# Optimization experiments

Hardware: AMD Instinct MI355X
Metric: run time of the kernel (lower is better)

Reference implementation:

```python
import jax, jax.numpy as jnp
import numpy as np

B, TQ, TKV, D, H = 2, 1024, 1024, 1024, 16
HD = D // H
BUCKETS, MAX_REL = 32, 128
SPAN = BUCKETS  # pos_ebd_size


def make_log_bucket_position(rel_pos, bucket_size, max_position):
    sign = jnp.sign(rel_pos)
    mid = bucket_size // 2
    abs_pos = jnp.where((rel_pos < mid) & (rel_pos > -mid), mid - 1, jnp.abs(rel_pos))
    log_pos = jnp.ceil(jnp.log(abs_pos.astype(jnp.float32) / mid)
                       / np.float32(np.log((max_position - 1) / mid)) * (mid - 1)) + mid
    return jnp.where(abs_pos <= mid, rel_pos, (log_pos * sign).astype(rel_pos.dtype))


def setup_inputs():
    key = jax.random.key(0)
    ks = jax.random.split(key, 12)
    s = 0.02
    f32 = jnp.float32
    return {
        "query_states": jax.random.normal(ks[0], (B, TQ, D), f32),
        "key_value_states": jax.random.normal(ks[1], (B, TKV, D), f32),
        "Wq": jax.random.normal(ks[2], (D, D), f32) * s, "bq": jnp.zeros((D,), f32),
        "Wk": jax.random.normal(ks[3], (D, D), f32) * s, "bk": jnp.zeros((D,), f32),
        "Wv": jax.random.normal(ks[4], (D, D), f32) * s, "bv": jnp.zeros((D,), f32),
        "Wo": jax.random.normal(ks[5], (D, D), f32) * s, "bo": jnp.zeros((D,), f32),
        "Wpk": jax.random.normal(ks[6], (D, D), f32) * s, "bpk": jnp.zeros((D,), f32),
        "Wpq": jax.random.normal(ks[7], (D, D), f32) * s, "bpq": jnp.zeros((D,), f32),
        "rel_emb": jax.random.normal(ks[8], (2 * SPAN, D), f32) * s,
        "ln_g": jnp.ones((D,), f32), "ln_b": jnp.zeros((D,), f32),
        "attention_mask": jnp.zeros((B, TKV), jnp.bool_),
    }


def reference(query_states, key_value_states, Wq, bq, Wk, bk, Wv, bv, Wo, bo,
              Wpk, bpk, Wpq, bpq, rel_emb, ln_g, ln_b, attention_mask):
    # projections -> [B,H,T,hd]
    q = (query_states @ Wq.T + bq).reshape(B, TQ, H, HD).transpose(0, 2, 1, 3)
    k = (key_value_states @ Wk.T + bk).reshape(B, TKV, H, HD).transpose(0, 2, 1, 3)
    v = (key_value_states @ Wv.T + bv).reshape(B, TKV, H, HD).transpose(0, 2, 1, 3)
    scale = jnp.sqrt(jnp.float32(HD * 3))  # scale_factor = 1 + c2p + p2c
    scores = jnp.einsum('bhqd,bhkd->bhqk', q, k) / scale

    # layer-normalized relative embeddings [2*SPAN, D]
    mu = rel_emb.mean(-1, keepdims=True)
    var = ((rel_emb - mu) ** 2).mean(-1, keepdims=True)
    re = (rel_emb - mu) * jax.lax.rsqrt(var + 1e-5) * ln_g + ln_b
    pos_k = (re @ Wpk.T + bpk).reshape(2 * SPAN, H, HD).transpose(1, 0, 2)  # [H,2S,hd]
    pos_q = (re @ Wpq.T + bpq).reshape(2 * SPAN, H, HD).transpose(1, 0, 2)

    rel = make_log_bucket_position(jnp.arange(TQ)[:, None] - jnp.arange(TKV)[None, :],
                                   BUCKETS, MAX_REL)                      # [Tq,Tkv]
    c2p_pos = jnp.clip(rel + SPAN, 0, 2 * SPAN - 1)
    p2c_pos = jnp.clip(-rel + SPAN, 0, 2 * SPAN - 1)
    pscale = jnp.sqrt(jnp.float32(HD * 2))

    # c2p: gather along relative-position axis
    c2p = jnp.einsum('bhqd,hpd->bhqp', q, pos_k)                          # [B,H,Tq,2S]
    iq = jnp.arange(TQ)[:, None]
    c2p_g = c2p[:, :, iq, c2p_pos]                                        # [B,H,Tq,Tkv]

    # p2c: gather then transpose (requires Tq == Tkv, as in original torch expand)
    p2c = jnp.einsum('bhkd,hpd->bhkp', k, pos_q)                          # [B,H,Tkv,2S]
    ik = jnp.arange(TKV)[:, None]
    p2c_g = p2c[:, :, ik, p2c_pos].transpose(0, 1, 3, 2)                  # [B,H,Tq,Tkv]

    scores = scores + c2p_g / pscale + p2c_g / pscale
    scores = jnp.where(attention_mask[:, None, None, :], -jnp.inf, scores)
    probs = jax.nn.softmax(scores.astype(jnp.float32), axis=-1).astype(q.dtype)

    ctx = jnp.einsum('bhqk,bhkd->bhqd', probs, v).transpose(0, 2, 1, 3).reshape(B, TQ, D)
    return ctx @ Wo.T + bo
```

## Files before the change

### kernel.cpp

```cpp
#include <hip/hip_runtime.h>
#include <hip/hip_bf16.h>
#include <math.h>

#define B   2
#define TQ  1024
#define TKV 1024
#define D   1024
#define H   16
#define HD  64
#define P   64
#define SPAN 32

#define NEG_INF (-3.0e38f)

typedef __attribute__((ext_vector_type(8))) short bf16x8;
typedef __attribute__((ext_vector_type(4))) float f32x4;
typedef unsigned short ushort_t;

static constexpr size_t QF_OFF   = 0;
static constexpr size_t CTX_OFF  = (size_t)2 * 1024 * 1024;
static constexpr size_t RE_OFF   = (size_t)4 * 1024 * 1024;
static constexpr size_t POSK_OFF = RE_OFF + (size_t)64 * 1024;
static constexpr size_t POSQ_OFF = POSK_OFF + (size_t)64 * 1024;
static constexpr size_t FLOATS_END = POSQ_OFF + (size_t)64 * 1024;
static constexpr size_t SHORT_BASE_BYTES = FLOATS_END * 4;
static constexpr size_t C2P_S = 0;
static constexpr size_t P2C_S = (size_t)2 * 1024 * 1024;
static constexpr size_t KH_S  = (size_t)4 * 1024 * 1024;
static constexpr size_t KL_S  = (size_t)6 * 1024 * 1024;
static constexpr size_t VTH_S = (size_t)8 * 1024 * 1024;
static constexpr size_t VTL_S = (size_t)10 * 1024 * 1024;
static constexpr size_t TAB_OFF_BYTES = SHORT_BASE_BYTES + (size_t)12 * 1024 * 1024 * 2;

__device__ __forceinline__ void split2(float x, unsigned short& h, unsigned short& l) {
  unsigned int u = __float_as_uint(x);
  h = (unsigned short)(u >> 16);
  float r = x - __uint_as_float(u & 0xffff0000u);
  unsigned int v = __float_as_uint(r);
  v += 0x7fffu + ((v >> 16) & 1u);
  l = (unsigned short)(v >> 16);
}

__device__ __forceinline__ unsigned short bf16rn(float x) {
  unsigned int v = __float_as_uint(x);
  v += 0x7fffu + ((v >> 16) & 1u);
  return (unsigned short)(v >> 16);
}

__device__ __forceinline__ float bf2f(unsigned short u) {
  return __uint_as_float(((unsigned int)u) << 16);
}

__global__ __launch_bounds__(256) void ln_kernel(const float* __restrict__ x,
    const float* __restrict__ g, const float* __restrict__ bta, float* __restrict__ out) {
  const int row = blockIdx.x;
  const float* xr = x + (size_t)row * D;
  const int tid = threadIdx.x;
  __shared__ float red[4];
  float s = 0.f;
  for (int i = tid; i < D; i += 256) s += xr[i];
  #pragma unroll
  for (int off = 32; off; off >>= 1) s += __shfl_down(s, off);
  if ((tid & 63) == 0) red[tid >> 6] = s;
  __syncthreads();
  float mu = (red[0] + red[1] + red[2] + red[3]) * (1.0f / D);
  __syncthreads();
  float vs = 0.f;
  for (int i = tid; i < D; i += 256) { float dd = xr[i] - mu; vs += dd * dd; }
  #pragma unroll
  for (int off = 32; off; off >>= 1) vs += __shfl_down(vs, off);
  if ((tid & 63) == 0) red[tid >> 6] = vs;
  __syncthreads();
  float var = (red[0] + red[1] + red[2] + red[3]) * (1.0f / D);
  float rs = rsqrtf(var + 1e-5f);
  for (int i = tid; i < D; i += 256)
    out[(size_t)row * D + i] = (xr[i] - mu) * rs * g[i] + bta[i];
}

__global__ void tab_kernel(unsigned char* __restrict__ tab) {
  int i = blockIdx.x * 256 + threadIdx.x;
  if (i >= 2047) return;
  int d = i - 1023;
  int ad = d < 0 ? -d : d;
  int bucket;
  if (ad <= 16) {
    bucket = d;
  } else {
    double x = log((double)ad / 16.0) / log(127.0 / 16.0) * 15.0;
    double xr = floor(x + 0.5);
    double xc = (fabs(x - xr) < 1e-9) ? xr : ceil(x);
    int li = (int)xc + 16;
    bucket = (d > 0) ? li : -li;
  }
  int t = bucket + SPAN;
  t = t < 0 ? 0 : (t > 63 ? 63 : t);
  tab[i] = (unsigned char)t;
}

__global__ __launch_bounds__(256) void gemm_pos(const float* __restrict__ A,
    const float* __restrict__ W0, const float* __restrict__ b0, float* __restrict__ C0,
    const float* __restrict__ W1, const float* __restrict__ b1, float* __restrict__ C1) {
  const float* W = blockIdx.z ? W1 : W0;
  const float* bias = blockIdx.z ? b1 : b0;
  float* C = blockIdx.z ? C1 : C0;

  __shared__ short sAh[64 * 32], sAl[64 * 32], sBh[64 * 32], sBl[64 * 32];
  const int t = threadIdx.x;
  const int bn = blockIdx.x * 64;
  const int wid = t >> 6, lane = t & 63;
  const int wr = wid >> 1, wc = wid & 1;
  const int fr = lane & 15, fo = (lane >> 4) * 8;
  const int srow = t >> 3, scol = (t & 7) * 4;

  f32x4 acc[2][2];
  #pragma unroll
  for (int i = 0; i < 2; i++)
    #pragma unroll
    for (int j = 0; j < 2; j++) acc[i][j] = (f32x4){0.f, 0.f, 0.f, 0.f};

  float4 rA[2], rW[2];
  auto ld = [&](int k0) {
    #pragma unroll
    for (int i = 0; i < 2; i++) {
      rA[i] = *(const float4*)&A[(size_t)(srow + 32 * i) * 1024 + k0 + scol];
      rW[i] = *(const float4*)&W[(size_t)(bn + srow + 32 * i) * 1024 + k0 + scol];
    }
  };
  ld(0);

  for (int k0 = 0; k0 < 1024; k0 += 32) {
    __syncthreads();
    #pragma unroll
    for (int i = 0; i < 2; i++) {
      int row = srow + 32 * i;
      unsigned short h0,h1,h2,h3,l0,l1,l2,l3;
      split2(rA[i].x,h0,l0); split2(rA[i].y,h1,l1); split2(rA[i].z,h2,l2); split2(rA[i].w,h3,l3);
      *(short4*)&sAh[row * 32 + scol] = make_short4((short)h0,(short)h1,(short)h2,(short)h3);
      *(short4*)&sAl[row * 32 + scol] = make_short4((short)l0,(short)l1,(short)l2,(short)l3);
      split2(rW[i].x,h0,l0); split2(rW[i].y,h1,l1); split2(rW[i].z,h2,l2); split2(rW[i].w,h3,l3);
      *(short4*)&sBh[row * 32 + scol] = make_short4((short)h0,(short)h1,(short)h2,(short)h3);
      *(short4*)&sBl[row * 32 + scol] = make_short4((short)l0,(short)l1,(short)l2,(short)l3);
    }
    if (k0 + 32 < 1024) ld(k0 + 32);
    __syncthreads();

    bf16x8 ah[2], al[2], bh[2], bl[2];
    #pragma unroll
    for (int mf = 0; mf < 2; mf++) {
      int r = (wr * 32 + mf * 16 + fr) * 32 + fo;
      ah[mf] = *(const bf16x8*)&sAh[r];
      al[mf] = *(const bf16x8*)&sAl[r];
    }
    #pragma unroll
    for (int nf = 0; nf < 2; nf++) {
      int r = (wc * 32 + nf * 16 + fr) * 32 + fo;
      bh[nf] = *(const bf16x8*)&sBh[r];
      bl[nf] = *(const bf16x8*)&sBl[r];
    }
    #pragma unroll
    for (int mf = 0; mf < 2; mf++)
      #pragma unroll
      for (int nf = 0; nf < 2; nf++) {
        acc[mf][nf] = __builtin_amdgcn_mfma_f32_16x16x32_bf16(ah[mf], bh[nf], acc[mf][nf], 0, 0, 0);
        acc[mf][nf] = __builtin_amdgcn_mfma_f32_16x16x32_bf16(ah[mf], bl[nf], acc[mf][nf], 0, 0, 0);
        acc[mf][nf] = __builtin_amdgcn_mfma_f32_16x16x32_bf16(al[mf], bh[nf], acc[mf][nf], 0, 0, 0);
      }
  }

  #pragma unroll
  for (int mf = 0; mf < 2; mf++) {
    int rbase = wr * 32 + mf * 16 + (lane >> 4) * 4;
    #pragma unroll
    for (int nf = 0; nf < 2; nf++) {
      int col = bn + wc * 32 + nf * 16 + fr;
      float bb = bias[col];
      #pragma unroll
      for (int r = 0; r < 4; r++)
        C[(size_t)(rbase + r) * 1024 + col] = acc[mf][nf][r] + bb;
    }
  }
}

__global__ __launch_bounds__(256) void gemm_split(
    const float* __restrict__ A0, const float* __restrict__ A1, const float* __restrict__ A2,
    const float* __restrict__ W0, const float* __restrict__ W1, const float* __restrict__ W2,
    const float* __restrict__ b0, const float* __restrict__ b1, const float* __restrict__ b2,
    float* __restrict__ Cf0,
    ushort_t* __restrict__ KH_, ushort_t* __restrict__ KL_,
    ushort_t* __restrict__ VH_, ushort_t* __restrict__ VL_,
    int M, int N, int K) {
  const int z = blockIdx.z;
  const float* A = (z == 0) ? A0 : (z == 1) ? A1 : A2;
  const float* W = (z == 0) ? W0 : (z == 1) ? W1 : W2;
  const float* bias = (z == 0) ? b0 : (z == 1) ? b1 : b2;

  __shared__ short sAhi[128 * 32];
  __shared__ short sAlo[128 * 32];
  __shared__ short sBhi[64 * 32];
  __shared__ short sBlo[64 * 32];

  const int t = threadIdx.x;
  const int bm = blockIdx.y * 128, bn = blockIdx.x * 64;
  const int wid = t >> 6, lane = t & 63;
  const int wr = wid >> 1, wc = wid & 1;
  const int fr = lane & 15, fo = (lane >> 4) * 8;

  f32x4 acc[4][2];
  #pragma unroll
  for (int i = 0; i < 4; i++)
    #pragma unroll
    for (int j = 0; j < 2; j++)
      acc[i][j] = (f32x4){0.f, 0.f, 0.f, 0.f};

  const int srow = t >> 3;
  const int scol = (t & 7) * 4;

  for (int k0 = 0; k0 < K; k0 += 32) {
    #pragma unroll
    for (int i = 0; i < 4; i++) {
      int row = srow + 32 * i;
      float4 a = *(const float4*)&A[(size_t)(bm + row) * K + k0 + scol];
      unsigned short h0, h1, h2, h3, l0, l1, l2, l3;
      split2(a.x, h0, l0); split2(a.y, h1, l1); split2(a.z, h2, l2); split2(a.w, h3, l3);
      *(short4*)&sAhi[row * 32 + scol] = make_short4((short)h0, (short)h1, (short)h2, (short)h3);
      *(short4*)&sAlo[row * 32 + scol] = make_short4((short)l0, (short)l1, (short)l2, (short)l3);
    }
    #pragma unroll
    for (int i = 0; i < 2; i++) {
      int row = srow + 32 * i;
      float4 a = *(const float4*)&W[(size_t)(bn + row) * K + k0 + scol];
      unsigned short h0, h1, h2, h3, l0, l1, l2, l3;
      split2(a.x, h0, l0); split2(a.y, h1, l1); split2(a.z, h2, l2); split2(a.w, h3, l3);
      *(short4*)&sBhi[row * 32 + scol] = make_short4((short)h0, (short)h1, (short)h2, (short)h3);
      *(short4*)&sBlo[row * 32 + scol] = make_short4((short)l0, (short)l1, (short)l2, (short)l3);
    }
    __syncthreads();

    bf16x8 ah[4], al[4], bh[2], bl[2];
    #pragma unroll
    for (int mf = 0; mf < 4; mf++) {
      int r = (wr * 64 + mf * 16 + fr) * 32 + fo;
      ah[mf] = *(const bf16x8*)&sAhi[r];
      al[mf] = *(const bf16x8*)&sAlo[r];
    }
    #pragma unroll
    for (int nf = 0; nf < 2; nf++) {
      int r = (wc * 32 + nf * 16 + fr) * 32 + fo;
      bh[nf] = *(const bf16x8*)&sBhi[r];
      bl[nf] = *(const bf16x8*)&sBlo[r];
    }
    #pragma unroll
    for (int mf = 0; mf < 4; mf++)
      #pragma unroll
      for (int nf = 0; nf < 2; nf++) {
        acc[mf][nf] = __builtin_amdgcn_mfma_f32_16x16x32_bf16(ah[mf], bh[nf], acc[mf][nf], 0, 0, 0);
        acc[mf][nf] = __builtin_amdgcn_mfma_f32_16x16x32_bf16(ah[mf], bl[nf], acc[mf][nf], 0, 0, 0);
        acc[mf][nf] = __builtin_amdgcn_mfma_f32_16x16x32_bf16(al[mf], bh[nf], acc[mf][nf], 0, 0, 0);
      }
    __syncthreads();
  }

  if (z == 0) {
    #pragma unroll
    for (int mf = 0; mf < 4; mf++) {
      int rbase = bm + wr * 64 + mf * 16 + (lane >> 4) * 4;
      #pragma unroll
      for (int nf = 0; nf < 2; nf++) {
        int col = bn + wc * 32 + nf * 16 + fr;
        float bb = bias[col];
        #pragma unroll
        for (int r = 0; r < 4; r++)
          Cf0[(size_t)(rbase + r) * N + col] = acc[mf][nf][r] + bb;
      }
    }
  } else if (z == 1) {
    #pragma unroll
    for (int mf = 0; mf < 4; mf++) {
      int rbase = bm + wr * 64 + mf * 16 + (lane >> 4) * 4;
      #pragma unroll
      for (int nf = 0; nf < 2; nf++) {
        int col = bn + wc * 32 + nf * 16 + fr;
        float bb = bias[col];
        #pragma unroll
        for (int r = 0; r < 4; r++) {
          unsigned short hh, ll;
          split2(acc[mf][nf][r] + bb, hh, ll);
          KH_[(size_t)(rbase + r) * N + col] = hh;
          KL_[(size_t)(rbase + r) * N + col] = ll;
        }
      }
    }
  } else {
    #pragma unroll
    for (int mf = 0; mf < 4; mf++) {
      int m0 = bm + wr * 64 + mf * 16 + (lane >> 4) * 4;
      int bb2 = m0 >> 10, t0 = m0 & 1023;
      #pragma unroll
      for (int nf = 0; nf < 2; nf++) {
        int col = bn + wc * 32 + nf * 16 + fr;
        int hh = col >> 6, dd = col & 63;
        float bvv = bias[col];
        unsigned short h4[4], l4[4];
        #pragma unroll
        for (int r = 0; r < 4; r++) split2(acc[mf][nf][r] + bvv, h4[r], l4[r]);
        size_t dst = (((size_t)bb2 * 16 + hh) * 64 + dd) * 1024 + t0;
        *(short4*)&VH_[dst] = make_short4((short)h4[0], (short)h4[1], (short)h4[2], (short)h4[3]);
        *(short4*)&VL_[dst] = make_short4((short)l4[0], (short)l4[1], (short)l4[2], (short)l4[3]);
      }
    }
  }
}

__global__ __launch_bounds__(256) void relproj_kernel(
    const float* __restrict__ X0, const float* __restrict__ P0, ushort_t* __restrict__ O0,
    const ushort_t* __restrict__ XH1, const ushort_t* __restrict__ XL1,
    const float* __restrict__ P1, ushort_t* __restrict__ O1) {
  const int z = blockIdx.z;
  const float* POS = z ? P1 : P0;
  ushort_t* out = z ? O1 : O0;
  const int bh = blockIdx.y, b = bh >> 4, h = bh & 15;
  const int t0 = blockIdx.x * 64;
  __shared__ __align__(16) float sx[64][68];
  __shared__ __align__(16) float sp[64][68];
  const int tid = threadIdx.x;
  for (int i = tid; i < 4096; i += 256) {
    int r = i >> 6, d = i & 63;
    size_t idx = ((size_t)b * TQ + t0 + r) * D + h * HD + d;
    sx[d][r] = z ? (bf2f(XH1[idx]) + bf2f(XL1[idx])) : X0[idx];
    sp[d][r] = POS[(size_t)r * D + h * HD + d];
  }
  __syncthreads();
  const int tx = tid & 15, ty = tid >> 4;
  float acc[4][4] = {};
  for (int d = 0; d < 64; d++) {
    float4 a4 = *(const float4*)&sx[d][ty * 4];
    float4 b4 = *(const float4*)&sp[d][tx * 4];
    float av[4] = {a4.x, a4.y, a4.z, a4.w};
    float bv[4] = {b4.x, b4.y, b4.z, b4.w};
    #pragma unroll
    for (int i = 0; i < 4; i++)
      #pragma unroll
      for (int j = 0; j < 4; j++)
        acc[i][j] += av[i] * bv[j];
  }
  const float inv_ps = 0.08838834764831845f;
  #pragma unroll
  for (int i = 0; i < 4; i++)
    #pragma unroll
    for (int j = 0; j < 4; j++)
      out[((size_t)bh * TQ + t0 + ty * 4 + i) * P + tx * 4 + j] = bf16rn(acc[i][j] * inv_ps);
}

__global__ __launch_bounds__(256) void attn_mfma(
    const float* __restrict__ qb,
    const ushort_t* __restrict__ KH, const ushort_t* __restrict__ KL,
    const ushort_t* __restrict__ VTH, const ushort_t* __restrict__ VTL,
    const ushort_t* __restrict__ c2p, const ushort_t* __restrict__ p2c,
    const unsigned char* __restrict__ mask, const unsigned char* __restrict__ tab,
    float* __restrict__ ctx) {
  const int flat = blockIdx.y * gridDim.x + blockIdx.x;
  const int nid = (flat & 7) * 64 + (flat >> 3);
  const int bh = nid >> 4, b = bh >> 4, h = bh & 15;
  const int q0 = (nid & 15) * 64;

  const int tid = threadIdx.x;
  const int wid = tid >> 6, lane = tid & 63;
  const int g = lane >> 4, fr = lane & 15;

  __shared__ __align__(16) short sKh[4096], sKl[4096], sVh[4096], sVl[4096];
  __shared__ __align__(16) ushort_t sc2p[64][72];
  __shared__ __align__(16) ushort_t sp2c[64][72];
  __shared__ unsigned char stab[2048];
  __shared__ unsigned char smask[64];

  bf16x8 qh[2], ql[2];
  {
    const int qrow = q0 + wid * 16 + fr;
    const float* qp = qb + ((size_t)b * TQ + qrow) * D + h * HD + g * 8;
    #pragma unroll
    for (int ks = 0; ks < 2; ks++) {
      float4 x0 = *(const float4*)(qp + ks * 32);
      float4 x1 = *(const float4*)(qp + ks * 32 + 4);
      float xs[8] = {x0.x, x0.y, x0.z, x0.w, x1.x, x1.y, x1.z, x1.w};
      bf16x8 th, tl;
      #pragma unroll
      for (int j = 0; j < 8; j++) {
        unsigned short hh, ll;
        split2(xs[j], hh, ll);
        th[j] = (short)hh; tl[j] = (short)ll;
      }
      qh[ks] = th; ql[ks] = tl;
    }
  }

  const int sr = tid >> 2;
  const int sj0 = tid & 3;
  const int smf = sr >> 4, sfr = sr & 15;
  const int cb = (tid & 3) * 16;

  {
    const ushort_t* cp = c2p + ((size_t)bh * TQ + q0 + sr) * P + cb;
    *(bf16x8*)&sc2p[sr][cb]     = *(const bf16x8*)cp;
    *(bf16x8*)&sc2p[sr][cb + 8] = *(const bf16x8*)(cp + 8);
  }
  for (int i = tid; i < 2047; i += 256) stab[i] = tab[i];

  f32x4 acc[4];
  #pragma unroll
  for (int nf = 0; nf < 4; nf++) acc[nf] = (f32x4){0.f, 0.f, 0.f, 0.f};
  float m_run = NEG_INF, l_run = 0.f;

  const float inv_s = 0.07216878364870323f;
  const int qloc = wid * 16 + fr;

  bf16x8 rKh[2], rKl[2], rVh[2], rVl[2], rP0, rP1;
  unsigned char rmask = 0;

  auto load_tile = [&](int kt) {
    const int k0n = kt * 64;
    const size_t kbase = ((size_t)b * TKV + k0n + sr) * D + h * HD;
    const size_t vbase = ((size_t)bh * HD + sr) * TKV + k0n;
    const ushort_t* pp = p2c + ((size_t)bh * TKV + k0n + sr) * P + cb;
    #pragma unroll
    for (int u = 0; u < 2; u++) {
      int jj = sj0 + u * 4;
      rKh[u] = *(const bf16x8*)(KH + kbase + jj * 8);
      rKl[u] = *(const bf16x8*)(KL + kbase + jj * 8);
      rVh[u] = *(const bf16x8*)(VTH + vbase + jj * 8);
      rVl[u] = *(const bf16x8*)(VTL + vbase + jj * 8);
    }
    rP0 = *(const bf16x8*)pp;
    rP1 = *(const bf16x8*)(pp + 8);
    if (tid < 64) rmask = mask[(size_t)b * TKV + k0n + tid];
  };

  load_tile(0);

  for (int kt = 0; kt < TKV / 64; kt++) {
    const int k0 = kt * 64;
    __syncthreads();
    #pragma unroll
    for (int u = 0; u < 2; u++) {
      int jj = sj0 + u * 4;
      int sub = smf * 8 + (jj >> 2) * 4 + (jj & 3);
      *(bf16x8*)&sKh[sub * 128 + sfr * 8] = rKh[u];
      *(bf16x8*)&sKl[sub * 128 + sfr * 8] = rKl[u];
      *(bf16x8*)&sVh[sub * 128 + sfr * 8] = rVh[u];
      *(bf16x8*)&sVl[sub * 128 + sfr * 8] = rVl[u];
    }
    *(bf16x8*)&sp2c[sr][cb]     = rP0;
    *(bf16x8*)&sp2c[sr][cb + 8] = rP1;
    if (tid < 64) smask[tid] = rmask;
    if (kt + 1 < TKV / 64) load_tile(kt + 1);
    __syncthreads();

    f32x4 st[4];
    #pragma unroll
    for (int mf = 0; mf < 4; mf++) st[mf] = (f32x4){0.f, 0.f, 0.f, 0.f};
    __builtin_amdgcn_s_setprio(1);
    #pragma unroll
    for (int mf = 0; mf < 4; mf++) {
      #pragma unroll
      for (int ks = 0; ks < 2; ks++) {
        bf16x8 kh = *(const bf16x8*)&sKh[(mf * 8 + ks * 4 + g) * 128 + fr * 8];
        bf16x8 kl = *(const bf16x8*)&sKl[(mf * 8 + ks * 4 + g) * 128 + fr * 8];
        st[mf] = __builtin_amdgcn_mfma_f32_16x16x32_bf16(kh, qh[ks], st[mf], 0, 0, 0);
        st[mf] = __builtin_amdgcn_mfma_f32_16x16x32_bf16(kh, ql[ks], st[mf], 0, 0, 0);
        st[mf] = __builtin_amdgcn_mfma_f32_16x16x32_bf16(kl, qh[ks], st[mf], 0, 0, 0);
      }
    }
    __builtin_amdgcn_s_setprio(0);

    const int dq = q0 + qloc - k0 + 1023;
    const ushort_t* c2prow = &sc2p[qloc][0];
    float pv[4][4];
    float lmax = NEG_INF;
    #pragma unroll
    for (int mf = 0; mf < 4; mf++) {
      #pragma unroll
      for (int rr = 0; rr < 4; rr++) {
        int kj = mf * 16 + g * 4 + rr;
        int tbi = stab[dq - kj];
        float v = st[mf][rr] * inv_s + (bf2f(c2prow[tbi]) + bf2f(sp2c[kj][tbi]));
        v = smask[kj] ? NEG_INF : v;
        pv[mf][rr] = v;
        lmax = fmaxf(lmax, v);
      }
    }
    lmax = fmaxf(lmax, __shfl_xor(lmax, 16));
    lmax = fmaxf(lmax, __shfl_xor(lmax, 32));
    if (!__all(lmax <= m_run)) {
      float mnew = fmaxf(m_run, lmax);
      float fac = __expf(m_run - mnew);
      m_run = mnew;
      l_run *= fac;
      float facr[4];
      #pragma unroll
      for (int rr = 0; rr < 4; rr++) facr[rr] = __shfl(fac, g * 4 + rr);
      #pragma unroll
      for (int nf = 0; nf < 4; nf++)
        #pragma unroll
        for (int rr = 0; rr < 4; rr++) acc[nf][rr] *= facr[rr];
    }
    float psum = 0.f;
    #pragma unroll
    for (int mf = 0; mf < 4; mf++)
      #pragma unroll
      for (int rr = 0; rr < 4; rr++) {
        float e = __expf(pv[mf][rr] - m_run);
        pv[mf][rr] = e;
        psum += e;
      }
    psum += __shfl_xor(psum, 16);
    psum += __shfl_xor(psum, 32);
    l_run += psum;

    bf16x8 pa[2];
    #pragma unroll
    for (int ks = 0; ks < 2; ks++) {
      bf16x8 t;
      #pragma unroll
      for (int j = 0; j < 8; j++) {
        int src = ((2 * (g & 1) + (j >> 2)) << 4) | fr;
        float v0 = __shfl(pv[2 * ks][j & 3], src);
        float v1 = __shfl(pv[2 * ks + 1][j & 3], src);
        float pvv = (g >> 1) ? v1 : v0;
        t[j] = (short)bf16rn(pvv);
      }
      pa[ks] = t;
    }

    __builtin_amdgcn_s_setprio(1);
    #pragma unroll
    for (int nf = 0; nf < 4; nf++) {
      #pragma unroll
      for (int ks = 0; ks < 2; ks++) {
        bf16x8 vh = *(const bf16x8*)&sVh[(nf * 8 + ks * 4 + g) * 128 + fr * 8];
        bf16x8 vl = *(const bf16x8*)&sVl[(nf * 8 + ks * 4 + g) * 128 + fr * 8];
        acc[nf] = __builtin_amdgcn_mfma_f32_16x16x32_bf16(pa[ks], vh, acc[nf], 0, 0, 0);
        acc[nf] = __builtin_amdgcn_mfma_f32_16x16x32_bf16(pa[ks], vl, acc[nf], 0, 0, 0);
      }
    }
    __builtin_amdgcn_s_setprio(0);
  }

  float invl[4];
  #pragma unroll
  for (int rr = 0; rr < 4; rr++) invl[rr] = 1.0f / __shfl(l_run, g * 4 + rr);
  #pragma unroll
  for (int nf = 0; nf < 4; nf++) {
    #pragma unroll
    for (int rr = 0; rr < 4; rr++) {
      int qrow = q0 + wid * 16 + g * 4 + rr;
      int dcol = h * HD + nf * 16 + fr;
      ctx[((size_t)b * TQ + qrow) * D + dcol] = acc[nf][rr] * invl[rr];
    }
  }
}

extern "C" void kernel_launch(void* const* d_in, const int* in_sizes, int n_in,
                              void* d_out, int out_size, void* d_ws, size_t ws_size,
                              hipStream_t stream) {
  const float* query = (const float*)d_in[0];
  const float* kv    = (const float*)d_in[1];
  const float* Wq  = (const float*)d_in[2];   const float* bq  = (const float*)d_in[3];
  const float* Wk  = (const float*)d_in[4];   const float* bk  = (const float*)d_in[5];
  const float* Wv  = (const float*)d_in[6];   const float* bv  = (const float*)d_in[7];
  const float* Wo  = (const float*)d_in[8];   const float* bo  = (const float*)d_in[9];
  const float* Wpk = (const float*)d_in[10];  const float* bpk = (const float*)d_in[11];
  const float* Wpq = (const float*)d_in[12];  const float* bpq = (const float*)d_in[13];
  const float* rel_emb = (const float*)d_in[14];
  const float* ln_g = (const float*)d_in[15];
  const float* ln_b = (const float*)d_in[16];
  const unsigned char* amask = (const unsigned char*)d_in[17];

  float* ws = (float*)d_ws;
  float* qbuf   = ws + QF_OFF;
  float* ctxbuf = ws + CTX_OFF;
  float* rebuf  = ws + RE_OFF;
  float* poskbuf = ws + POSK_OFF;
  float* posqbuf = ws + POSQ_OFF;
  ushort_t* sbase = (ushort_t*)((char*)d_ws + SHORT_BASE_BYTES);
  ushort_t* c2pbuf = sbase + C2P_S;
  ushort_t* p2cbuf = sbase + P2C_S;
  ushort_t* KH  = sbase + KH_S;
  ushort_t* KL  = sbase + KL_S;
  ushort_t* VTH = sbase + VTH_S;
  ushort_t* VTL = sbase + VTL_S;
  unsigned char* tab = (unsigned char*)d_ws + TAB_OFF_BYTES;

  ln_kernel<<<64, 256, 0, stream>>>(rel_emb, ln_g, ln_b, rebuf);
  tab_kernel<<<8, 256, 0, stream>>>(tab);
  gemm_pos<<<dim3(16, 1, 2), 256, 0, stream>>>(rebuf, Wpk, bpk, poskbuf, Wpq, bpq, posqbuf);
  gemm_split<<<dim3(16, 16, 3), 256, 0, stream>>>(
      query, kv, kv,  Wq, Wk, Wv,  bq, bk, bv,
      qbuf, KH, KL, VTH, VTL, 2048, 1024, 1024);
  relproj_kernel<<<dim3(16, 32, 2), 256, 0, stream>>>(
      qbuf, poskbuf, c2pbuf, KH, KL, posqbuf, p2cbuf);
  attn_mfma<<<dim3(16, 32), 256, 0, stream>>>(qbuf, KH, KL, VTH, VTL,
                                              c2pbuf, p2cbuf, amask, tab, ctxbuf);
  gemm_split<<<dim3(16, 16, 1), 256, 0, stream>>>(
      ctxbuf, ctxbuf, ctxbuf,  Wo, Wo, Wo,  bo, bo, bo,
      (float*)d_out, nullptr, nullptr, nullptr, nullptr, 2048, 1024, 1024);
}
```

Baseline: 229.0 us.

## Prefetch GEMM tiles into registers, add split-bf16 output GEMM, fast-path far tiles

The split-bf16 GEMM now prefetches the next K-slice of A and W into registers while the current slice is in shared memory, which also removes one barrier per iteration. The attention kernel writes its context directly as hi/lo bf16 halves. A new gemm_out kernel with a 64x64 tile consumes those halves, so the activation split is no longer redone and the output GEMM gets more blocks. In attention, tiles whose relative distance lies fully outside the bucket span use a constant c2p/p2c column instead of per-element table lookups. The cost is extra register pressure from the prefetch and an additional shared-memory barrier at attention start.

```diff
diff --git a/kernel.cpp b/kernel.cpp
--- a/kernel.cpp
+++ b/kernel.cpp
@@ -18,19 +18,20 @@
 typedef unsigned short ushort_t;
 
 static constexpr size_t QF_OFF   = 0;
-static constexpr size_t CTX_OFF  = (size_t)2 * 1024 * 1024;
-static constexpr size_t RE_OFF   = (size_t)4 * 1024 * 1024;
+static constexpr size_t RE_OFF   = (size_t)2 * 1024 * 1024;
 static constexpr size_t POSK_OFF = RE_OFF + (size_t)64 * 1024;
 static constexpr size_t POSQ_OFF = POSK_OFF + (size_t)64 * 1024;
 static constexpr size_t FLOATS_END = POSQ_OFF + (size_t)64 * 1024;
 static constexpr size_t SHORT_BASE_BYTES = FLOATS_END * 4;
-static constexpr size_t C2P_S = 0;
-static constexpr size_t P2C_S = (size_t)2 * 1024 * 1024;
-static constexpr size_t KH_S  = (size_t)4 * 1024 * 1024;
-static constexpr size_t KL_S  = (size_t)6 * 1024 * 1024;
-static constexpr size_t VTH_S = (size_t)8 * 1024 * 1024;
-static constexpr size_t VTL_S = (size_t)10 * 1024 * 1024;
-static constexpr size_t TAB_OFF_BYTES = SHORT_BASE_BYTES + (size_t)12 * 1024 * 1024 * 2;
+static constexpr size_t C2P_S  = 0;
+static constexpr size_t P2C_S  = (size_t)2 * 1024 * 1024;
+static constexpr size_t KH_S   = (size_t)4 * 1024 * 1024;
+static constexpr size_t KL_S   = (size_t)6 * 1024 * 1024;
+static constexpr size_t VTH_S  = (size_t)8 * 1024 * 1024;
+static constexpr size_t VTL_S  = (size_t)10 * 1024 * 1024;
+static constexpr size_t CTXH_S = (size_t)12 * 1024 * 1024;
+static constexpr size_t CTXL_S = (size_t)14 * 1024 * 1024;
+static constexpr size_t TAB_OFF_BYTES = SHORT_BASE_BYTES + (size_t)16 * 1024 * 1024 * 2;
 
 __device__ __forceinline__ void split2(float x, unsigned short& h, unsigned short& l) {
   unsigned int u = __float_as_uint(x);
@@ -215,25 +216,36 @@
   const int srow = t >> 3;
   const int scol = (t & 7) * 4;
 
+  float4 rA[4], rW[2];
+  auto ld = [&](int k0) {
+    #pragma unroll
+    for (int i = 0; i < 4; i++)
+      rA[i] = *(const float4*)&A[(size_t)(bm + srow + 32 * i) * K + k0 + scol];
+    #pragma unroll
+    for (int i = 0; i < 2; i++)
+      rW[i] = *(const float4*)&W[(size_t)(bn + srow + 32 * i) * K + k0 + scol];
+  };
+  ld(0);
+
   for (int k0 = 0; k0 < K; k0 += 32) {
+    __syncthreads();
     #pragma unroll
     for (int i = 0; i < 4; i++) {
       int row = srow + 32 * i;
-      float4 a = *(const float4*)&A[(size_t)(bm + row) * K + k0 + scol];
       unsigned short h0, h1, h2, h3, l0, l1, l2, l3;
-      split2(a.x, h0, l0); split2(a.y, h1, l1); split2(a.z, h2, l2); split2(a.w, h3, l3);
+      split2(rA[i].x, h0, l0); split2(rA[i].y, h1, l1); split2(rA[i].z, h2, l2); split2(rA[i].w, h3, l3);
       *(short4*)&sAhi[row * 32 + scol] = make_short4((short)h0, (short)h1, (short)h2, (short)h3);
       *(short4*)&sAlo[row * 32 + scol] = make_short4((short)l0, (short)l1, (short)l2, (short)l3);
     }
     #pragma unroll
     for (int i = 0; i < 2; i++) {
       int row = srow + 32 * i;
-      float4 a = *(const float4*)&W[(size_t)(bn + row) * K + k0 + scol];
       unsigned short h0, h1, h2, h3, l0, l1, l2, l3;
-      split2(a.x, h0, l0); split2(a.y, h1, l1); split2(a.z, h2, l2); split2(a.w, h3, l3);
+      split2(rW[i].x, h0, l0); split2(rW[i].y, h1, l1); split2(rW[i].z, h2, l2); split2(rW[i].w, h3, l3);
       *(short4*)&sBhi[row * 32 + scol] = make_short4((short)h0, (short)h1, (short)h2, (short)h3);
       *(short4*)&sBlo[row * 32 + scol] = make_short4((short)l0, (short)l1, (short)l2, (short)l3);
     }
+    if (k0 + 32 < K) ld(k0 + 32);
     __syncthreads();
 
     bf16x8 ah[4], al[4], bh[2], bl[2];
@@ -257,7 +269,6 @@
         acc[mf][nf] = __builtin_amdgcn_mfma_f32_16x16x32_bf16(ah[mf], bl[nf], acc[mf][nf], 0, 0, 0);
         acc[mf][nf] = __builtin_amdgcn_mfma_f32_16x16x32_bf16(al[mf], bh[nf], acc[mf][nf], 0, 0, 0);
       }
-    __syncthreads();
   }
 
   if (z == 0) {
@@ -307,6 +318,87 @@
         *(short4*)&VH_[dst] = make_short4((short)h4[0], (short)h4[1], (short)h4[2], (short)h4[3]);
         *(short4*)&VL_[dst] = make_short4((short)l4[0], (short)l4[1], (short)l4[2], (short)l4[3]);
       }
+    }
+  }
+}
+
+__global__ __launch_bounds__(256) void gemm_out(
+    const ushort_t* __restrict__ AH, const ushort_t* __restrict__ AL,
+    const float* __restrict__ W, const float* __restrict__ bias, float* __restrict__ C) {
+  __shared__ short sAh[64 * 32], sAl[64 * 32], sBh[64 * 32], sBl[64 * 32];
+  const int t = threadIdx.x;
+  const int bm = blockIdx.y * 64, bn = blockIdx.x * 64;
+  const int wid = t >> 6, lane = t & 63;
+  const int wr = wid >> 1, wc = wid & 1;
+  const int fr = lane & 15, fo = (lane >> 4) * 8;
+  const int arow = t >> 2, achk = (t & 3) * 8;
+  const int srow = t >> 3, scol = (t & 7) * 4;
+
+  f32x4 acc[2][2];
+  #pragma unroll
+  for (int i = 0; i < 2; i++)
+    #pragma unroll
+    for (int j = 0; j < 2; j++) acc[i][j] = (f32x4){0.f, 0.f, 0.f, 0.f};
+
+  bf16x8 rAH, rAL;
+  float4 rW[2];
+  auto ld = [&](int k0) {
+    rAH = *(const bf16x8*)&AH[(size_t)(bm + arow) * 1024 + k0 + achk];
+    rAL = *(const bf16x8*)&AL[(size_t)(bm + arow) * 1024 + k0 + achk];
+    #pragma unroll
+    for (int i = 0; i < 2; i++)
+      rW[i] = *(const float4*)&W[(size_t)(bn + srow + 32 * i) * 1024 + k0 + scol];
+  };
+  ld(0);
+
+  for (int k0 = 0; k0 < 1024; k0 += 32) {
+    __syncthreads();
+    *(bf16x8*)&sAh[arow * 32 + achk] = rAH;
+    *(bf16x8*)&sAl[arow * 32 + achk] = rAL;
+    #pragma unroll
+    for (int i = 0; i < 2; i++) {
+      int row = srow + 32 * i;
+      unsigned short h0,h1,h2,h3,l0,l1,l2,l3;
+      split2(rW[i].x,h0,l0); split2(rW[i].y,h1,l1); split2(rW[i].z,h2,l2); split2(rW[i].w,h3,l3);
+      *(short4*)&sBh[row * 32 + scol] = make_short4((short)h0,(short)h1,(short)h2,(short)h3);
+      *(short4*)&sBl[row * 32 + scol] = make_short4((short)l0,(short)l1,(short)l2,(short)l3);
+    }
+    if (k0 + 32 < 1024) ld(k0 + 32);
+    __syncthreads();
+
+    bf16x8 ah[2], al[2], bh[2], bl[2];
+    #pragma unroll
+    for (int mf = 0; mf < 2; mf++) {
+      int r = (wr * 32 + mf * 16 + fr) * 32 + fo;
+      ah[mf] = *(const bf16x8*)&sAh[r];
+      al[mf] = *(const bf16x8*)&sAl[r];
+    }
+    #pragma unroll
+    for (int nf = 0; nf < 2; nf++) {
+      int r = (wc * 32 + nf * 16 + fr) * 32 + fo;
+      bh[nf] = *(const bf16x8*)&sBh[r];
+      bl[nf] = *(const bf16x8*)&sBl[r];
+    }
+    #pragma unroll
+    for (int mf = 0; mf < 2; mf++)
+      #pragma unroll
+      for (int nf = 0; nf < 2; nf++) {
+        acc[mf][nf] = __builtin_amdgcn_mfma_f32_16x16x32_bf16(ah[mf], bh[nf], acc[mf][nf], 0, 0, 0);
+        acc[mf][nf] = __builtin_amdgcn_mfma_f32_16x16x32_bf16(ah[mf], bl[nf], acc[mf][nf], 0, 0, 0);
+        acc[mf][nf] = __builtin_amdgcn_mfma_f32_16x16x32_bf16(al[mf], bh[nf], acc[mf][nf], 0, 0, 0);
+      }
+  }
+
+  #pragma unroll
+  for (int mf = 0; mf < 2; mf++) {
+    int rbase = bm + wr * 32 + mf * 16 + (lane >> 4) * 4;
+    #pragma unroll
+    for (int nf = 0; nf < 2; nf++) {
+      int col = bn + wc * 32 + nf * 16 + fr;
+      float bb = bias[col];
+      #pragma unroll
+      for (int r = 0; r < 4; r++)
+        C[(size_t)(rbase + r) * 1024 + col] = acc[mf][nf][r] + bb;
     }
   }
 }
@@ -357,7 +449,7 @@
     const ushort_t* __restrict__ VTH, const ushort_t* __restrict__ VTL,
     const ushort_t* __restrict__ c2p, const ushort_t* __restrict__ p2c,
     const unsigned char* __restrict__ mask, const unsigned char* __restrict__ tab,
-    float* __restrict__ ctx) {
+    ushort_t* __restrict__ CTXH, ushort_t* __restrict__ CTXL) {
   const int flat = blockIdx.y * gridDim.x + blockIdx.x;
   const int nid = (flat & 7) * 64 + (flat >> 3);
   const int bh = nid >> 4, b = bh >> 4, h = bh & 15;
@@ -397,6 +489,7 @@
   const int sj0 = tid & 3;
   const int smf = sr >> 4, sfr = sr & 15;
   const int cb = (tid & 3) * 16;
+  const int qloc = wid * 16 + fr;
 
   {
     const ushort_t* cp = c2p + ((size_t)bh * TQ + q0 + sr) * P + cb;
@@ -404,6 +497,9 @@
     *(bf16x8*)&sc2p[sr][cb + 8] = *(const bf16x8*)(cp + 8);
   }
   for (int i = tid; i < 2047; i += 256) stab[i] = tab[i];
+  __syncthreads();
+  const float c2p0  = bf2f(sc2p[qloc][0]);
+  const float c2p63 = bf2f(sc2p[qloc][63]);
 
   f32x4 acc[4];
   #pragma unroll
@@ -411,7 +507,6 @@
   float m_run = NEG_INF, l_run = 0.f;
 
   const float inv_s = 0.07216878364870323f;
-  const int qloc = wid * 16 + fr;
 
   bf16x8 rKh[2], rKl[2], rVh[2], rVl[2], rP0, rP1;
   unsigned char rmask = 0;
@@ -471,20 +566,37 @@
     }
     __builtin_amdgcn_s_setprio(0);
 
-    const int dq = q0 + qloc - k0 + 1023;
-    const ushort_t* c2prow = &sc2p[qloc][0];
+    const int dtile = q0 - k0;
     float pv[4][4];
     float lmax = NEG_INF;
-    #pragma unroll
-    for (int mf = 0; mf < 4; mf++) {
-      #pragma unroll
-      for (int rr = 0; rr < 4; rr++) {
-        int kj = mf * 16 + g * 4 + rr;
-        int tbi = stab[dq - kj];
-        float v = st[mf][rr] * inv_s + (bf2f(c2prow[tbi]) + bf2f(sp2c[kj][tbi]));
-        v = smask[kj] ? NEG_INF : v;
-        pv[mf][rr] = v;
-        lmax = fmaxf(lmax, v);
+    if (dtile >= 192 || dtile <= -192) {
+      const int C = (dtile >= 192) ? 63 : 0;
+      const float cbias = (dtile >= 192) ? c2p63 : c2p0;
+      #pragma unroll
+      for (int mf = 0; mf < 4; mf++) {
+        #pragma unroll
+        for (int rr = 0; rr < 4; rr++) {
+          int kj = mf * 16 + g * 4 + rr;
+          float v = st[mf][rr] * inv_s + (cbias + bf2f(sp2c[kj][C]));
+          v = smask[kj] ? NEG_INF : v;
+          pv[mf][rr] = v;
+          lmax = fmaxf(lmax, v);
+        }
+      }
+    } else {
+      const int dq = q0 + qloc - k0 + 1023;
+      const ushort_t* c2prow = &sc2p[qloc][0];
+      #pragma unroll
+      for (int mf = 0; mf < 4; mf++) {
+        #pragma unroll
+        for (int rr = 0; rr < 4; rr++) {
+          int kj = mf * 16 + g * 4 + rr;
+          int tbi = stab[dq - kj];
+          float v = st[mf][rr] * inv_s + (bf2f(c2prow[tbi]) + bf2f(sp2c[kj][tbi]));
+          v = smask[kj] ? NEG_INF : v;
+          pv[mf][rr] = v;
+          lmax = fmaxf(lmax, v);
+        }
       }
     }
     lmax = fmaxf(lmax, __shfl_xor(lmax, 16));
@@ -553,7 +665,11 @@
     for (int rr = 0; rr < 4; rr++) {
       int qrow = q0 + wid * 16 + g * 4 + rr;
       int dcol = h * HD + nf * 16 + fr;
-      ctx[((size_t)b * TQ + qrow) * D + dcol] = acc[nf][rr] * invl[rr];
+      size_t idx = ((size_t)b * TQ + qrow) * D + dcol;
+      unsigned short hh, ll;
+      split2(acc[nf][rr] * invl[rr], hh, ll);
+      CTXH[idx] = hh;
+      CTXL[idx] = ll;
     }
   }
 }
@@ -576,17 +692,18 @@
 
   float* ws = (float*)d_ws;
   float* qbuf   = ws + QF_OFF;
-  float* ctxbuf = ws + CTX_OFF;
   float* rebuf  = ws + RE_OFF;
   float* poskbuf = ws + POSK_OFF;
   float* posqbuf = ws + POSQ_OFF;
   ushort_t* sbase = (ushort_t*)((char*)d_ws + SHORT_BASE_BYTES);
   ushort_t* c2pbuf = sbase + C2P_S;
   ushort_t* p2cbuf = sbase + P2C_S;
-  ushort_t* KH  = sbase + KH_S;
-  ushort_t* KL  = sbase + KL_S;
-  ushort_t* VTH = sbase + VTH_S;
-  ushort_t* VTL = sbase + VTL_S;
+  ushort_t* KH   = sbase + KH_S;
+  ushort_t* KL   = sbase + KL_S;
+  ushort_t* VTH  = sbase + VTH_S;
+  ushort_t* VTL  = sbase + VTL_S;
+  ushort_t* CTXH = sbase + CTXH_S;
+  ushort_t* CTXL = sbase + CTXL_S;
   unsigned char* tab = (unsigned char*)d_ws + TAB_OFF_BYTES;
 
   ln_kernel<<<64, 256, 0, stream>>>(rel_emb, ln_g, ln_b, rebuf);
@@ -598,8 +715,6 @@
   relproj_kernel<<<dim3(16, 32, 2), 256, 0, stream>>>(
       qbuf, poskbuf, c2pbuf, KH, KL, posqbuf, p2cbuf);
   attn_mfma<<<dim3(16, 32), 256, 0, stream>>>(qbuf, KH, KL, VTH, VTL,
-                                              c2pbuf, p2cbuf, amask, tab, ctxbuf);
-  gemm_split<<<dim3(16, 16, 1), 256, 0, stream>>>(
-      ctxbuf, ctxbuf, ctxbuf,  Wo, Wo, Wo,  bo, bo, bo,
-      (float*)d_out, nullptr, nullptr, nullptr, nullptr, 2048, 1024, 1024);
-}
+                                              c2pbuf, p2cbuf, amask, tab, CTXH, CTXL);
+  gemm_out<<<dim3(16, 32), 256, 0, stream>>>(CTXH, CTXL, Wo, bo, (float*)d_out);
+}
```

New measurement: 201.0 us. -12.2%, faster.
